# Optimization experiments

Measured on AMD Instinct MI355X. Metric: run time of the kernel, lower is better.

Reference implementation:

```python
import jax, jax.numpy as jnp
import numpy as np

MASK_VALUE = -1e30


def setup_inputs() -> dict:
    key = jax.random.key(0)
    ks = jax.random.split(key, 8)
    B, N, M, D = 64, 1024, 128, 256
    c = jax.random.normal(ks[0], (B, N, D), dtype=jnp.float32)
    q = jax.random.normal(ks[1], (B, M, D), dtype=jnp.float32)
    c_mask = jax.random.randint(ks[2], (B, N), 0, 2, dtype=jnp.int32)
    q_mask = jax.random.randint(ks[3], (B, M), 0, 2, dtype=jnp.int32)
    w0 = jax.random.normal(ks[4], (D, 1), dtype=jnp.float32) * 0.06  # glorot-ish scale
    w1 = jax.random.normal(ks[5], (D, 1), dtype=jnp.float32) * 0.06
    wm = jax.random.normal(ks[6], (D,), dtype=jnp.float32) * 0.06
    bias = jnp.zeros((M,), dtype=jnp.float32)
    return {"c": c, "q": q, "c_mask": c_mask, "q_mask": q_mask,
            "w0": w0, "w1": w1, "wm": wm, "bias": bias}


def reference(c, q, c_mask, q_mask, w0, w1, wm, bias):
    # Trilinear similarity S[b,i,j] = c.w0 + q.w1 + sum_d c*wm*q + bias[j]
    sub0 = jnp.einsum('bnd,do->bno', c, w0)              # (B,N,1)
    sub1 = jnp.einsum('bmd,do->bom', q, w1)              # (B,1,M)
    sub2 = jnp.einsum('bnd,d,bmd->bnm', c, wm, q)        # (B,N,M)
    S = sub0 + sub1 + sub2 + bias                        # bias broadcast over last axis
    qm = q_mask.astype(jnp.float32)[:, None, :]          # (B,1,M)
    cm = c_mask.astype(jnp.float32)[:, :, None]          # (B,N,1)
    S_ = jax.nn.softmax(S + MASK_VALUE * (1.0 - qm), axis=-1)   # row softmax over query
    S_T = jnp.swapaxes(jax.nn.softmax(S + MASK_VALUE * (1.0 - cm), axis=1), 1, 2)  # (B,M,N)
    c2q = jnp.matmul(S_, q)                              # (B,N,D)
    q2c = jnp.matmul(jnp.matmul(S_, S_T), c)             # (B,N,D)
    return jnp.concatenate([c, c2q, c * c2q, c * q2c], axis=-1)  # (B,N,4D)
```

## Files before the change

kernel.cpp:

```cpp
#include <hip/hip_runtime.h>
#include <cfloat>

#define BB 64
#define NN 1024
#define MM 128
#define DD 256
#define MASKV (-1e30f)

typedef __attribute__((ext_vector_type(8))) short bf16x8;
typedef __attribute__((ext_vector_type(16))) float f32x16;

__device__ __forceinline__ unsigned short f2bf(float x) {
  union { float f; unsigned int u; } v; v.f = x;
  unsigned int r = v.u + 0x7fffu + ((v.u >> 16) & 1u);
  return (unsigned short)(r >> 16);
}
__device__ __forceinline__ float bf2f(unsigned short h) {
  union { float f; unsigned int u; } v; v.u = ((unsigned int)h) << 16;
  return v.f;
}
__device__ __forceinline__ void split8(const float* xs, uint4* hv, uint4* lv) {
  unsigned hp[4], lp[4];
  #pragma unroll
  for (int p = 0; p < 4; p++) {
    unsigned short h0 = f2bf(xs[2 * p]), h1 = f2bf(xs[2 * p + 1]);
    unsigned short g0 = f2bf(xs[2 * p] - bf2f(h0));
    unsigned short g1 = f2bf(xs[2 * p + 1] - bf2f(h1));
    hp[p] = (unsigned)h0 | ((unsigned)h1 << 16);
    lp[p] = (unsigned)g0 | ((unsigned)g1 << 16);
  }
  *hv = make_uint4(hp[0], hp[1], hp[2], hp[3]);
  *lv = make_uint4(lp[0], lp[1], lp[2], lp[3]);
}
__device__ __forceinline__ bf16x8 u2b(uint4 u) {
  union { uint4 a; bf16x8 b; } x; x.a = u; return x.b;
}

__global__ __launch_bounds__(256) void k_dots(
    const float* __restrict__ c, const float* __restrict__ q,
    const int* __restrict__ qmask,
    const float* __restrict__ w0, const float* __restrict__ w1,
    const float* __restrict__ bias,
    float* __restrict__ sub0, float* __restrict__ qtermM) {
  int wave = (blockIdx.x * blockDim.x + threadIdx.x) >> 6;
  int lane = threadIdx.x & 63;
  const int total = BB * NN + BB * MM;
  if (wave >= total) return;
  const float* row;
  const float* w;
  if (wave < BB * NN) { row = c + (size_t)wave * DD; w = w0; }
  else                { row = q + (size_t)(wave - BB * NN) * DD; w = w1; }
  float4 v  = *(const float4*)(row + lane * 4);
  float4 wv = *(const float4*)(w   + lane * 4);
  float s = v.x * wv.x + v.y * wv.y + v.z * wv.z + v.w * wv.w;
  #pragma unroll
  for (int off = 32; off > 0; off >>= 1) s += __shfl_xor(s, off, 64);
  if (lane == 0) {
    if (wave < BB * NN) {
      sub0[wave] = s;
    } else {
      int r = wave - BB * NN;
      int m = r & (MM - 1);
      qtermM[r] = s + bias[m] + (qmask[r] ? 0.0f : MASKV);
    }
  }
}

__global__ __launch_bounds__(256) void k_zero(float* __restrict__ p) {
  p[blockIdx.x * 256 + threadIdx.x] = 0.0f;
}

__global__ __launch_bounds__(256) void k_pack(
    const float* __restrict__ src, int nparts, int pstride,
    const float* __restrict__ colsum,
    unsigned short* __restrict__ dsth, unsigned short* __restrict__ dstl) {
  const int dchunk = blockIdx.x;
  const int b = blockIdx.y;
  const int t = threadIdx.x;
  const int col = t & 31;
  const int lh = (t >> 5) & 1;
  const int wq = t >> 6;
  const float* sb = src + (size_t)b * MM * DD;
  #pragma unroll
  for (int i = 0; i < 4; i++) {
    int u = i * 4 + wq;
    int f_local = u >> 3, ks = u & 7;
    int f = dchunk * 2 + f_local;
    int d = f * 32 + col;
    float ys[8];
    #pragma unroll
    for (int j = 0; j < 8; j++) {
      int m = ks * 16 + lh * 8 + j;
      float v = sb[(size_t)m * DD + d];
      for (int p = 1; p < nparts; p++) v += sb[(size_t)p * pstride + (size_t)m * DD + d];
      if (colsum) v *= 1.0f / colsum[b * MM + m];
      ys[j] = v;
    }
    uint4 hv, lv;
    split8(ys, &hv, &lv);
    size_t off = (size_t)b * 32768 + (size_t)(((f * 8 + ks) * 64) + lh * 32 + col) * 8;
    *(uint4*)(dsth + off) = hv;
    *(uint4*)(dstl + off) = lv;
  }
}

__global__ __launch_bounds__(256) void k_score(
    const float* __restrict__ c, const float* __restrict__ q,
    const int* __restrict__ cmask, const float* __restrict__ wm,
    const float* __restrict__ sub0, const float* __restrict__ qtermM,
    float* __restrict__ S_,
    unsigned short* __restrict__ EThi, unsigned short* __restrict__ ETlo,
    float* __restrict__ colsum) {
  __shared__ unsigned short cwh[128 * 64];
  __shared__ unsigned short cwl[128 * 64];
  __shared__ unsigned short qhi[128 * 64];
  __shared__ unsigned short qlo[128 * 64];
  const int b = blockIdx.y;
  const int n0 = blockIdx.x * 128;
  const int t = threadIdx.x;
  const int w = t >> 6;
  const int l = t & 63;
  const int l31 = l & 31;
  const int lh = l >> 5;

  f32x16 acc[4];
  #pragma unroll
  for (int mb = 0; mb < 4; mb++)
    #pragma unroll
    for (int i = 0; i < 16; i++) acc[mb][i] = 0.0f;

  for (int k0 = 0; k0 < DD; k0 += 64) {
    __syncthreads();
    #pragma unroll
    for (int g = 0; g < 4; g++) {
      int lin = t + g * 256;
      int row = lin >> 3;
      int kg  = (lin & 7) * 8;
      unsigned boff = (unsigned)(row * 128 + ((kg * 2) ^ ((row & 7) << 4)));
      float4 w0v = *(const float4*)(wm + k0 + kg);
      float4 w1v = *(const float4*)(wm + k0 + kg + 4);
      const float* cp = c + (size_t)(b * NN + n0 + row) * DD + k0 + kg;
      float4 a0 = *(const float4*)cp;
      float4 a1 = *(const float4*)(cp + 4);
      float xs[8] = {a0.x * w0v.x, a0.y * w0v.y, a0.z * w0v.z, a0.w * w0v.w,
                     a1.x * w1v.x, a1.y * w1v.y, a1.z * w1v.z, a1.w * w1v.w};
      uint4 hv, lv;
      split8(xs, &hv, &lv);
      *(uint4*)((char*)cwh + boff) = hv;
      *(uint4*)((char*)cwl + boff) = lv;
      const float* qp = q + (size_t)(b * MM + row) * DD + k0 + kg;
      float4 b0 = *(const float4*)qp;
      float4 b1 = *(const float4*)(qp + 4);
      float ys[8] = {b0.x, b0.y, b0.z, b0.w, b1.x, b1.y, b1.z, b1.w};
      split8(ys, &hv, &lv);
      *(uint4*)((char*)qhi + boff) = hv;
      *(uint4*)((char*)qlo + boff) = lv;
    }
    __syncthreads();
    #pragma unroll
    for (int ks = 0; ks < 64; ks += 16) {
      int ak = ks + lh * 8;
      unsigned arow = (unsigned)(w * 32 + l31);
      unsigned aoff = arow * 128 + (((unsigned)(ak * 2)) ^ ((arow & 7) << 4));
      bf16x8 ah = *(const bf16x8*)((const char*)cwh + aoff);
      bf16x8 al = *(const bf16x8*)((const char*)cwl + aoff);
      #pragma unroll
      for (int mb = 0; mb < 4; mb++) {
        unsigned brow = (unsigned)(mb * 32 + l31);
        unsigned boff2 = brow * 128 + (((unsigned)(ak * 2)) ^ ((brow & 7) << 4));
        bf16x8 bh = *(const bf16x8*)((const char*)qhi + boff2);
        bf16x8 bl = *(const bf16x8*)((const char*)qlo + boff2);
        acc[mb] = __builtin_amdgcn_mfma_f32_32x32x16_bf16(ah, bh, acc[mb], 0, 0, 0);
        acc[mb] = __builtin_amdgcn_mfma_f32_32x32x16_bf16(ah, bl, acc[mb], 0, 0, 0);
        acc[mb] = __builtin_amdgcn_mfma_f32_32x32x16_bf16(al, bh, acc[mb], 0, 0, 0);
      }
    }
  }

  float qt[4];
  #pragma unroll
  for (int mb = 0; mb < 4; mb++) qt[mb] = qtermM[b * MM + mb * 32 + l31];

  float ps[4] = {0.f, 0.f, 0.f, 0.f};
  #pragma unroll
  for (int g = 0; g < 4; g++) {
    float evg[4][4];
    #pragma unroll
    for (int j = 0; j < 4; j++) {
      int r = 4 * g + j;
      int row = j + 8 * g + 4 * lh;
      int gn = n0 + w * 32 + row;
      float s0m = sub0[b * NN + gn] + (cmask[b * NN + gn] ? 0.0f : MASKV);
      float x[4];
      float vmax = -FLT_MAX;
      #pragma unroll
      for (int mb = 0; mb < 4; mb++) { x[mb] = acc[mb][r] + qt[mb]; vmax = fmaxf(vmax, x[mb]); }
      #pragma unroll
      for (int off = 16; off > 0; off >>= 1) vmax = fmaxf(vmax, __shfl_xor(vmax, off, 64));
      float e[4];
      float vsum = 0.0f;
      #pragma unroll
      for (int mb = 0; mb < 4; mb++) { e[mb] = __expf(x[mb] - vmax); vsum += e[mb]; }
      #pragma unroll
      for (int off = 16; off > 0; off >>= 1) vsum += __shfl_xor(vsum, off, 64);
      float inv = 1.0f / vsum;
      size_t base = (size_t)(b * NN + gn) * MM + l31;
      #pragma unroll
      for (int mb = 0; mb < 4; mb++) {
        S_[base + mb * 32] = e[mb] * inv;
        float Ev = __expf(acc[mb][r] + s0m);
        evg[mb][j] = Ev;
        ps[mb] += Ev;
      }
    }
    #pragma unroll
    for (int mb = 0; mb < 4; mb++) {
      unsigned short h[4], lo[4];
      #pragma unroll
      for (int j = 0; j < 4; j++) {
        h[j] = f2bf(evg[mb][j]);
        lo[j] = f2bf(evg[mb][j] - bf2f(h[j]));
      }
      size_t off = (size_t)(b * MM + mb * 32 + l31) * NN + n0 + w * 32 + 8 * g + 4 * lh;
      *(uint2*)(EThi + off) = make_uint2((unsigned)h[0] | ((unsigned)h[1] << 16),
                                         (unsigned)h[2] | ((unsigned)h[3] << 16));
      *(uint2*)(ETlo + off) = make_uint2((unsigned)lo[0] | ((unsigned)lo[1] << 16),
                                         (unsigned)lo[2] | ((unsigned)lo[3] << 16));
    }
  }
  #pragma unroll
  for (int mb = 0; mb < 4; mb++) {
    ps[mb] += __shfl_xor(ps[mb], 32, 64);
    if (lh == 0) atomicAdd(&colsum[b * MM + mb * 32 + l31], ps[mb]);
  }
}

__global__ __launch_bounds__(512) void k_colA(
    const unsigned short* __restrict__ EThi, const unsigned short* __restrict__ ETlo,
    const float* __restrict__ c, float* __restrict__ Apart) {
  const int p = blockIdx.x;
  const int b = blockIdx.y;
  const int t = threadIdx.x;
  const int w = t >> 6;
  const int l = t & 63;
  const int l31 = l & 31, lh = l >> 5;
  const int d = w * 32 + l31;

  f32x16 acc[4];
  #pragma unroll
  for (int mf = 0; mf < 4; mf++)
    #pragma unroll
    for (int i = 0; i < 16; i++) acc[mf][i] = 0.0f;

  const float* cb = c + (size_t)b * NN * DD + d;
  const size_t etb = (size_t)b * MM * NN + (size_t)p * 256 + lh * 8;

  for (int ks = 0; ks < 16; ks++) {
    int nb = p * 256 + ks * 16 + lh * 8;
    float ys[8];
    #pragma unroll
    for (int j = 0; j < 8; j++) ys[j] = cb[(size_t)(nb + j) * DD];
    uint4 hv, lv;
    split8(ys, &hv, &lv);
    bf16x8 ah = u2b(hv), al = u2b(lv);
    #pragma unroll
    for (int mf = 0; mf < 4; mf++) {
      size_t eoff = etb + (size_t)(mf * 32 + l31) * NN + ks * 16;
      bf16x8 bh = *(const bf16x8*)(EThi + eoff);
      bf16x8 bl = *(const bf16x8*)(ETlo + eoff);
      acc[mf] = __builtin_amdgcn_mfma_f32_32x32x16_bf16(ah, bh, acc[mf], 0, 0, 0);
      acc[mf] = __builtin_amdgcn_mfma_f32_32x32x16_bf16(ah, bl, acc[mf], 0, 0, 0);
      acc[mf] = __builtin_amdgcn_mfma_f32_32x32x16_bf16(al, bh, acc[mf], 0, 0, 0);
    }
  }

  float* ap = Apart + (size_t)p * (BB * MM * DD);
  #pragma unroll
  for (int mf = 0; mf < 4; mf++) {
    size_t rowb = (size_t)(b * MM + mf * 32 + l31) * DD + w * 32 + 4 * lh;
    #pragma unroll
    for (int g = 0; g < 4; g++) {
      float4 o = make_float4(acc[mf][4 * g + 0], acc[mf][4 * g + 1],
                             acc[mf][4 * g + 2], acc[mf][4 * g + 3]);
      *(float4*)(ap + rowb + 8 * g) = o;
    }
  }
}

__global__ __launch_bounds__(512) void k_out(
    const float* __restrict__ c, const float* __restrict__ S_,
    const unsigned short* __restrict__ qfh, const unsigned short* __restrict__ qfl,
    const unsigned short* __restrict__ afh, const unsigned short* __restrict__ afl,
    float* __restrict__ out) {
  const int b = blockIdx.y;
  const int n0 = blockIdx.x * 64;
  const int t = threadIdx.x;
  const int w = t >> 6;
  const int l = t & 63;
  const int l31 = l & 31;
  const int lh = l >> 5;
  const int grp = w >> 2;
  const int wi = w & 3;
  const int nf = wi & 1;
  const int fd0 = (wi >> 1) * 4;

  const unsigned short* Bh = grp ? afh : qfh;
  const unsigned short* Bl = grp ? afl : qfl;
  const size_t fb = (size_t)b * 32768;

  f32x16 acc[4];
  #pragma unroll
  for (int df = 0; df < 4; df++)
    #pragma unroll
    for (int i = 0; i < 16; i++) acc[df][i] = 0.0f;

  const float* srow = S_ + (size_t)(b * NN + n0 + nf * 32 + l31) * MM + lh * 8;

  #pragma unroll 2
  for (int ks = 0; ks < 8; ks++) {
    float4 s0 = *(const float4*)(srow + ks * 16);
    float4 s1 = *(const float4*)(srow + ks * 16 + 4);
    float xs[8] = {s0.x, s0.y, s0.z, s0.w, s1.x, s1.y, s1.z, s1.w};
    uint4 hv, lv;
    split8(xs, &hv, &lv);
    bf16x8 ah = u2b(hv), al = u2b(lv);
    #pragma unroll
    for (int df = 0; df < 4; df++) {
      int f = fd0 + df;
      size_t off = fb + (size_t)(((f * 8 + ks) * 64) + l) * 8;
      bf16x8 bh = *(const bf16x8*)(Bh + off);
      bf16x8 bl = *(const bf16x8*)(Bl + off);
      acc[df] = __builtin_amdgcn_mfma_f32_32x32x16_bf16(ah, bh, acc[df], 0, 0, 0);
      acc[df] = __builtin_amdgcn_mfma_f32_32x32x16_bf16(ah, bl, acc[df], 0, 0, 0);
      acc[df] = __builtin_amdgcn_mfma_f32_32x32x16_bf16(al, bh, acc[df], 0, 0, 0);
    }
  }

  #pragma unroll
  for (int df = 0; df < 4; df++) {
    int d = (fd0 + df) * 32 + l31;
    #pragma unroll
    for (int r = 0; r < 16; r++) {
      int row = (r & 3) + 8 * (r >> 2) + 4 * lh;
      int gn = n0 + nf * 32 + row;
      float v = acc[df][r];
      float cv = c[(size_t)(b * NN + gn) * DD + d];
      size_t ob = (size_t)(b * NN + gn) * (4 * DD) + d;
      if (grp == 0) {
        out[ob]            = cv;
        out[ob + DD]       = v;
        out[ob + 2 * DD]   = cv * v;
      } else {
        out[ob + 3 * DD]   = cv * v;
      }
    }
  }
}

extern "C" void kernel_launch(void* const* d_in, const int* in_sizes, int n_in,
                              void* d_out, int out_size, void* d_ws, size_t ws_size,
                              hipStream_t stream) {
  const float* c     = (const float*)d_in[0];
  const float* q     = (const float*)d_in[1];
  const int*   cmask = (const int*)d_in[2];
  const int*   qmask = (const int*)d_in[3];
  const float* w0    = (const float*)d_in[4];
  const float* w1    = (const float*)d_in[5];
  const float* wm    = (const float*)d_in[6];
  const float* bias  = (const float*)d_in[7];
  float* out = (float*)d_out;
  float* ws  = (float*)d_ws;

  float* S_     = ws;
  unsigned short* EThi = (unsigned short*)(ws + 8388608);
  unsigned short* ETlo = (unsigned short*)(ws + 12582912);
  float* Apart  = ws + 16777216;
  unsigned short* qfh = (unsigned short*)(ws + 25165824);
  unsigned short* qfl = (unsigned short*)(ws + 26214400);
  unsigned short* afh = (unsigned short*)(ws + 27262976);
  unsigned short* afl = (unsigned short*)(ws + 28311552);
  float* sub0   = ws + 29360128;
  float* qtermM = ws + 29425664;
  float* colsum = ws + 29433856;

  k_dots<<<18432, 256, 0, stream>>>(c, q, qmask, w0, w1, bias, sub0, qtermM);
  k_zero<<<32, 256, 0, stream>>>(colsum);
  k_pack<<<dim3(4, BB), 256, 0, stream>>>(q, 1, 0, nullptr, qfh, qfl);
  k_score<<<dim3(8, BB), 256, 0, stream>>>(c, q, cmask, wm, sub0, qtermM, S_, EThi, ETlo, colsum);
  k_colA<<<dim3(4, BB), 512, 0, stream>>>(EThi, ETlo, c, Apart);
  k_pack<<<dim3(4, BB), 256, 0, stream>>>(Apart, 4, BB * MM * DD, colsum, afh, afl);
  k_out<<<dim3(16, BB), 512, 0, stream>>>(c, S_, qfh, qfl, afh, afl, out);
}
```

Measured before the change: 560.2 us.

## Stage E^T through LDS for coalesced stores, widen pack and out grids

k_score now writes its exp-score tiles (hi/lo bf16) into swizzled shared memory and then copies them out with full 16-byte coalesced row stores, replacing scattered 8-byte global writes. The pack kernel is split into q and A variants, each running with four times as many blocks and one unit of work per wave. k_out is restructured so each wave computes both the c2q and q2c products for one 32-wide d slice over 32 rows. This doubles its grid and writes all four output segments from the same thread. The extra LDS round-trip and syncs in k_score trade against the cost of the uncoalesced global writes.

```diff
diff --git a/kernel.cpp b/kernel.cpp
--- a/kernel.cpp
+++ b/kernel.cpp
@@ -70,38 +70,48 @@
   p[blockIdx.x * 256 + threadIdx.x] = 0.0f;
 }
 
-__global__ __launch_bounds__(256) void k_pack(
-    const float* __restrict__ src, int nparts, int pstride,
-    const float* __restrict__ colsum,
+__global__ __launch_bounds__(256) void k_pack_q(
+    const float* __restrict__ q,
     unsigned short* __restrict__ dsth, unsigned short* __restrict__ dstl) {
-  const int dchunk = blockIdx.x;
   const int b = blockIdx.y;
-  const int t = threadIdx.x;
-  const int col = t & 31;
-  const int lh = (t >> 5) & 1;
-  const int wq = t >> 6;
-  const float* sb = src + (size_t)b * MM * DD;
-  #pragma unroll
-  for (int i = 0; i < 4; i++) {
-    int u = i * 4 + wq;
-    int f_local = u >> 3, ks = u & 7;
-    int f = dchunk * 2 + f_local;
-    int d = f * 32 + col;
-    float ys[8];
-    #pragma unroll
-    for (int j = 0; j < 8; j++) {
-      int m = ks * 16 + lh * 8 + j;
-      float v = sb[(size_t)m * DD + d];
-      for (int p = 1; p < nparts; p++) v += sb[(size_t)p * pstride + (size_t)m * DD + d];
-      if (colsum) v *= 1.0f / colsum[b * MM + m];
-      ys[j] = v;
-    }
-    uint4 hv, lv;
-    split8(ys, &hv, &lv);
-    size_t off = (size_t)b * 32768 + (size_t)(((f * 8 + ks) * 64) + lh * 32 + col) * 8;
-    *(uint4*)(dsth + off) = hv;
-    *(uint4*)(dstl + off) = lv;
-  }
+  const int u = blockIdx.x * 4 + (threadIdx.x >> 6);
+  const int f = u >> 3, ks = u & 7;
+  const int l = threadIdx.x & 63;
+  const int l31 = l & 31, lh = l >> 5;
+  const float* sb = q + (size_t)b * MM * DD + (size_t)(ks * 16 + lh * 8) * DD + f * 32 + l31;
+  float ys[8];
+  #pragma unroll
+  for (int j = 0; j < 8; j++) ys[j] = sb[(size_t)j * DD];
+  uint4 hv, lv;
+  split8(ys, &hv, &lv);
+  size_t off = (size_t)b * 32768 + (size_t)(u * 64 + l) * 8;
+  *(uint4*)(dsth + off) = hv;
+  *(uint4*)(dstl + off) = lv;
+}
+
+__global__ __launch_bounds__(256) void k_pack_a(
+    const float* __restrict__ Apart, const float* __restrict__ colsum,
+    unsigned short* __restrict__ dsth, unsigned short* __restrict__ dstl) {
+  const int b = blockIdx.y;
+  const int u = blockIdx.x * 4 + (threadIdx.x >> 6);
+  const int f = u >> 3, ks = u & 7;
+  const int l = threadIdx.x & 63;
+  const int l31 = l & 31, lh = l >> 5;
+  const int m0 = ks * 16 + lh * 8;
+  const size_t P = (size_t)BB * MM * DD;
+  const float* sb = Apart + (size_t)b * MM * DD + (size_t)m0 * DD + f * 32 + l31;
+  float ys[8];
+  #pragma unroll
+  for (int j = 0; j < 8; j++) {
+    float v = sb[(size_t)j * DD] + sb[P + (size_t)j * DD] +
+              sb[2 * P + (size_t)j * DD] + sb[3 * P + (size_t)j * DD];
+    ys[j] = v * (1.0f / colsum[b * MM + m0 + j]);
+  }
+  uint4 hv, lv;
+  split8(ys, &hv, &lv);
+  size_t off = (size_t)b * 32768 + (size_t)(u * 64 + l) * 8;
+  *(uint4*)(dsth + off) = hv;
+  *(uint4*)(dstl + off) = lv;
 }
 
 __global__ __launch_bounds__(256) void k_score(
@@ -111,10 +121,11 @@
     float* __restrict__ S_,
     unsigned short* __restrict__ EThi, unsigned short* __restrict__ ETlo,
     float* __restrict__ colsum) {
-  __shared__ unsigned short cwh[128 * 64];
-  __shared__ unsigned short cwl[128 * 64];
-  __shared__ unsigned short qhi[128 * 64];
-  __shared__ unsigned short qlo[128 * 64];
+  __shared__ unsigned short smem[32768];
+  unsigned short* cwh = smem;
+  unsigned short* cwl = smem + 8192;
+  unsigned short* qhi = smem + 16384;
+  unsigned short* qlo = smem + 24576;
   const int b = blockIdx.y;
   const int n0 = blockIdx.x * 128;
   const int t = threadIdx.x;
@@ -177,6 +188,10 @@
     }
   }
 
+  unsigned short* eth = smem;
+  unsigned short* etl = smem + 16384;
+  __syncthreads();
+
   float qt[4];
   #pragma unroll
   for (int mb = 0; mb < 4; mb++) qt[mb] = qtermM[b * MM + mb * 32 + l31];
@@ -213,25 +228,45 @@
         ps[mb] += Ev;
       }
     }
+    int nloc = w * 32 + 8 * g + 4 * lh;
     #pragma unroll
     for (int mb = 0; mb < 4; mb++) {
+      int m = mb * 32 + l31;
       unsigned short h[4], lo[4];
       #pragma unroll
       for (int j = 0; j < 4; j++) {
         h[j] = f2bf(evg[mb][j]);
         lo[j] = f2bf(evg[mb][j] - bf2f(h[j]));
       }
-      size_t off = (size_t)(b * MM + mb * 32 + l31) * NN + n0 + w * 32 + 8 * g + 4 * lh;
-      *(uint2*)(EThi + off) = make_uint2((unsigned)h[0] | ((unsigned)h[1] << 16),
-                                         (unsigned)h[2] | ((unsigned)h[3] << 16));
-      *(uint2*)(ETlo + off) = make_uint2((unsigned)lo[0] | ((unsigned)lo[1] << 16),
-                                         (unsigned)lo[2] | ((unsigned)lo[3] << 16));
+      unsigned addr = (unsigned)(m * 256 + ((nloc * 2) ^ ((m & 15) << 4)));
+      *(uint2*)((char*)eth + addr) = make_uint2(
+          (unsigned)h[0] | ((unsigned)h[1] << 16),
+          (unsigned)h[2] | ((unsigned)h[3] << 16));
+      *(uint2*)((char*)etl + addr) = make_uint2(
+          (unsigned)lo[0] | ((unsigned)lo[1] << 16),
+          (unsigned)lo[2] | ((unsigned)lo[3] << 16));
     }
   }
   #pragma unroll
   for (int mb = 0; mb < 4; mb++) {
     ps[mb] += __shfl_xor(ps[mb], 32, 64);
     if (lh == 0) atomicAdd(&colsum[b * MM + mb * 32 + l31], ps[mb]);
+  }
+
+  __syncthreads();
+  {
+    int chunk = t & 15;
+    int mrow0 = t >> 4;
+    #pragma unroll
+    for (int it = 0; it < 8; it++) {
+      int m = it * 16 + mrow0;
+      int sw = (chunk * 16) ^ ((m & 15) << 4);
+      uint4 vh = *(const uint4*)((const char*)eth + m * 256 + sw);
+      uint4 vl = *(const uint4*)((const char*)etl + m * 256 + sw);
+      size_t gb = (size_t)(b * MM + m) * NN + n0 + chunk * 8;
+      *(uint4*)(EThi + gb) = vh;
+      *(uint4*)(ETlo + gb) = vl;
+    }
   }
 }
 
@@ -287,36 +322,27 @@
   }
 }
 
-__global__ __launch_bounds__(512) void k_out(
+__global__ __launch_bounds__(512, 4) void k_out(
     const float* __restrict__ c, const float* __restrict__ S_,
     const unsigned short* __restrict__ qfh, const unsigned short* __restrict__ qfl,
     const unsigned short* __restrict__ afh, const unsigned short* __restrict__ afl,
     float* __restrict__ out) {
   const int b = blockIdx.y;
-  const int n0 = blockIdx.x * 64;
+  const int n0 = blockIdx.x * 32;
   const int t = threadIdx.x;
   const int w = t >> 6;
   const int l = t & 63;
   const int l31 = l & 31;
   const int lh = l >> 5;
-  const int grp = w >> 2;
-  const int wi = w & 3;
-  const int nf = wi & 1;
-  const int fd0 = (wi >> 1) * 4;
-
-  const unsigned short* Bh = grp ? afh : qfh;
-  const unsigned short* Bl = grp ? afl : qfl;
-  const size_t fb = (size_t)b * 32768;
-
-  f32x16 acc[4];
-  #pragma unroll
-  for (int df = 0; df < 4; df++)
-    #pragma unroll
-    for (int i = 0; i < 16; i++) acc[df][i] = 0.0f;
-
-  const float* srow = S_ + (size_t)(b * NN + n0 + nf * 32 + l31) * MM + lh * 8;
-
-  #pragma unroll 2
+
+  f32x16 acc0, acc1;
+  #pragma unroll
+  for (int i = 0; i < 16; i++) { acc0[i] = 0.0f; acc1[i] = 0.0f; }
+
+  const float* srow = S_ + (size_t)(b * NN + n0 + l31) * MM + lh * 8;
+  const size_t fo = (size_t)b * 32768 + (size_t)(w * 8 * 64 + l) * 8;
+
+  #pragma unroll
   for (int ks = 0; ks < 8; ks++) {
     float4 s0 = *(const float4*)(srow + ks * 16);
     float4 s1 = *(const float4*)(srow + ks * 16 + 4);
@@ -324,36 +350,31 @@
     uint4 hv, lv;
     split8(xs, &hv, &lv);
     bf16x8 ah = u2b(hv), al = u2b(lv);
-    #pragma unroll
-    for (int df = 0; df < 4; df++) {
-      int f = fd0 + df;
-      size_t off = fb + (size_t)(((f * 8 + ks) * 64) + l) * 8;
-      bf16x8 bh = *(const bf16x8*)(Bh + off);
-      bf16x8 bl = *(const bf16x8*)(Bl + off);
-      acc[df] = __builtin_amdgcn_mfma_f32_32x32x16_bf16(ah, bh, acc[df], 0, 0, 0);
-      acc[df] = __builtin_amdgcn_mfma_f32_32x32x16_bf16(ah, bl, acc[df], 0, 0, 0);
-      acc[df] = __builtin_amdgcn_mfma_f32_32x32x16_bf16(al, bh, acc[df], 0, 0, 0);
-    }
-  }
-
-  #pragma unroll
-  for (int df = 0; df < 4; df++) {
-    int d = (fd0 + df) * 32 + l31;
-    #pragma unroll
-    for (int r = 0; r < 16; r++) {
-      int row = (r & 3) + 8 * (r >> 2) + 4 * lh;
-      int gn = n0 + nf * 32 + row;
-      float v = acc[df][r];
-      float cv = c[(size_t)(b * NN + gn) * DD + d];
-      size_t ob = (size_t)(b * NN + gn) * (4 * DD) + d;
-      if (grp == 0) {
-        out[ob]            = cv;
-        out[ob + DD]       = v;
-        out[ob + 2 * DD]   = cv * v;
-      } else {
-        out[ob + 3 * DD]   = cv * v;
-      }
-    }
+    size_t off = fo + (size_t)(ks * 64) * 8;
+    bf16x8 qh = *(const bf16x8*)(qfh + off);
+    bf16x8 ql = *(const bf16x8*)(qfl + off);
+    bf16x8 vh = *(const bf16x8*)(afh + off);
+    bf16x8 vl = *(const bf16x8*)(afl + off);
+    acc0 = __builtin_amdgcn_mfma_f32_32x32x16_bf16(ah, qh, acc0, 0, 0, 0);
+    acc0 = __builtin_amdgcn_mfma_f32_32x32x16_bf16(ah, ql, acc0, 0, 0, 0);
+    acc0 = __builtin_amdgcn_mfma_f32_32x32x16_bf16(al, qh, acc0, 0, 0, 0);
+    acc1 = __builtin_amdgcn_mfma_f32_32x32x16_bf16(ah, vh, acc1, 0, 0, 0);
+    acc1 = __builtin_amdgcn_mfma_f32_32x32x16_bf16(ah, vl, acc1, 0, 0, 0);
+    acc1 = __builtin_amdgcn_mfma_f32_32x32x16_bf16(al, vh, acc1, 0, 0, 0);
+  }
+
+  const int d = w * 32 + l31;
+  #pragma unroll
+  for (int r = 0; r < 16; r++) {
+    int row = (r & 3) + 8 * (r >> 2) + 4 * lh;
+    int gn = n0 + row;
+    float cv = c[(size_t)(b * NN + gn) * DD + d];
+    size_t ob = (size_t)(b * NN + gn) * (4 * DD) + d;
+    float v1 = acc0[r], v3 = acc1[r];
+    out[ob]          = cv;
+    out[ob + DD]     = v1;
+    out[ob + 2 * DD] = cv * v1;
+    out[ob + 3 * DD] = cv * v3;
   }
 }
 
@@ -385,9 +406,9 @@
 
   k_dots<<<18432, 256, 0, stream>>>(c, q, qmask, w0, w1, bias, sub0, qtermM);
   k_zero<<<32, 256, 0, stream>>>(colsum);
-  k_pack<<<dim3(4, BB), 256, 0, stream>>>(q, 1, 0, nullptr, qfh, qfl);
+  k_pack_q<<<dim3(16, BB), 256, 0, stream>>>(q, qfh, qfl);
   k_score<<<dim3(8, BB), 256, 0, stream>>>(c, q, cmask, wm, sub0, qtermM, S_, EThi, ETlo, colsum);
   k_colA<<<dim3(4, BB), 512, 0, stream>>>(EThi, ETlo, c, Apart);
-  k_pack<<<dim3(4, BB), 256, 0, stream>>>(Apart, 4, BB * MM * DD, colsum, afh, afl);
-  k_out<<<dim3(16, BB), 512, 0, stream>>>(c, S_, qfh, qfl, afh, afl, out);
-}
+  k_pack_a<<<dim3(16, BB), 256, 0, stream>>>(Apart, colsum, afh, afl);
+  k_out<<<dim3(32, BB), 512, 0, stream>>>(c, S_, qfh, qfl, afh, afl, out);
+}
```

Measured after the change: 487.2 us. 13.0% less time.
